# Kernel optimization log

Hardware: AMD Instinct MI355X
Metric: run time of the kernel (lower is better)

The kernel has to match this reference:

```python
import jax, jax.numpy as jnp
import numpy as np

EPS = 1e-10

def setup_inputs() -> dict:
    key = jax.random.key(0)
    k1, k2 = jax.random.split(key)
    B, N, D = 8, 4096, 3
    points_ref = jax.random.normal(k1, (B, N, D), dtype=jnp.float32)
    points = jax.random.normal(k2, (B, N, D), dtype=jnp.float32)
    return {"points_ref": points_ref, "points": points, "nn_size": 16}

def _knn(points_ref, K):
    # pairwise squared distances (B,N,N)
    sq = jnp.sum(points_ref * points_ref, axis=-1)
    d2 = sq[:, :, None] + sq[:, None, :] - 2.0 * jnp.einsum('bnd,bmd->bnm', points_ref, points_ref)
    _, idx = jax.lax.top_k(-d2, K)  # nearest first; idx: (B,N,K)
    return idx

def reference(points_ref, points, nn_size):
    K = nn_size + 1
    knn_idx = _knn(points_ref, K)[:, :, 1:]  # drop self -> (B,N,nn_size)
    gather = jax.vmap(lambda p, i: p[i])  # (N,D),(N,K) -> (N,K,D)
    group_ref = gather(points_ref, knn_idx)           # (B,N,K,D)
    group_pred = gather(points, knn_idx)              # (B,N,K,D)
    dist_ref = jnp.linalg.norm(group_ref - points_ref[:, :, None, :], axis=-1)  # (B,N,K)
    dist = jnp.linalg.norm(group_pred - points[:, :, None, :], axis=-1)         # (B,N,K)
    stretch = jnp.maximum(dist / (dist_ref + EPS) - 1.0, 0.0)
    return jnp.mean(stretch)
```

## Files before the change

### kernel.cpp

```cpp
#include <hip/hip_runtime.h>

#define NPTS  4096
#define KNN   16
#define K1    17
#define NBLK  64
#define CELLS 4096
#define EPSF  1e-10f

__device__ __forceinline__ unsigned umin_(unsigned a, unsigned b) { return a < b ? a : b; }
__device__ __forceinline__ unsigned umax_(unsigned a, unsigned b) { return a < b ? b : a; }

#define DPP_XOR1(v)  ((unsigned)__builtin_amdgcn_update_dpp(0, (int)(v), 0xB1, 0xF, 0xF, true))
#define DPP_XOR2(v)  ((unsigned)__builtin_amdgcn_update_dpp(0, (int)(v), 0x4E, 0xF, 0xF, true))
#define SWZ_XOR(v,J) ((unsigned)__builtin_amdgcn_ds_swizzle((int)(v), ((J) << 10) | 0x1F))
#define DPP_SHR1(v)  ((unsigned)__builtin_amdgcn_update_dpp(0, (int)(v), 0x111, 0xF, 0xF, true))
#define DPPF_SHR(vf, CTRL) __uint_as_float((unsigned)__builtin_amdgcn_update_dpp(0, (int)__float_as_uint(vf), CTRL, 0xF, 0xF, true))
#define LXOR1(v)  DPP_XOR1(v)
#define LXOR2(v)  DPP_XOR2(v)
#define LXOR4(v)  SWZ_XOR(v, 4)
#define LXOR8(v)  SWZ_XOR(v, 8)
#define LXOR16(v) SWZ_XOR(v, 16)
#define LXOR32(v) ((unsigned)__shfl_xor((int)(v), 32))

#define BSTEP(K, XORF) do {                                                   \
    unsigned o1_ = XORF(arr), o2_ = XORF(bk);                                 \
    bool tm_ = (((lane & (J_)) == 0) == ((lane & (K)) == 0));                 \
    unsigned mn1_ = umin_(arr, o1_), mx1_ = umax_(arr, o1_);                  \
    unsigned mn2_ = umin_(bk, o2_),  mx2_ = umax_(bk, o2_);                   \
    arr = tm_ ? mn1_ : mx1_; bk = tm_ ? mn2_ : mx2_;                          \
} while (0)

__device__ __forceinline__ unsigned sp4(int v) {
    unsigned x = (unsigned)v;
    return (x & 1u) | ((x & 2u) << 2) | ((x & 4u) << 4) | ((x & 8u) << 6);
}

__global__ __launch_bounds__(1024) void sort_kernel(
    const float* __restrict__ pref,
    float4* __restrict__ wxyzw, int* __restrict__ widx, float4* __restrict__ wbb)
{
    __shared__ unsigned hist[CELLS];
    __shared__ unsigned short cells[NPTS];
    __shared__ unsigned wofs[16];
    const int tid  = threadIdx.x;
    const int lane = tid & 63, w = tid >> 6;
    const int b = blockIdx.x;
    const float* prb = pref + (size_t)b * NPTS * 3;
    const size_t base = (size_t)b * NPTS;

    for (int t = tid; t < CELLS; t += 1024) hist[t] = 0u;
    __syncthreads();

    for (int p = tid; p < NPTS; p += 1024) {
        float x = prb[3 * p + 0], y = prb[3 * p + 1], z = prb[3 * p + 2];
        int cx = min(15, max(0, (int)((x + 4.0f) * 2.0f)));
        int cy = min(15, max(0, (int)((y + 4.0f) * 2.0f)));
        int cz = min(15, max(0, (int)((z + 4.0f) * 2.0f)));
        unsigned m = sp4(cx) | (sp4(cy) << 1) | (sp4(cz) << 2);
        cells[p] = (unsigned short)m;
        atomicAdd(&hist[m], 1u);
    }
    __syncthreads();

    unsigned l0 = hist[4 * tid + 0], l1 = hist[4 * tid + 1];
    unsigned l2 = hist[4 * tid + 2], l3 = hist[4 * tid + 3];
    unsigned s = l0 + l1 + l2 + l3;
    unsigned run = s;
#pragma unroll
    for (int d = 1; d < 64; d <<= 1) {
        unsigned o = __shfl_up(run, d);
        if (lane >= d) run += o;
    }
    if (lane == 63) wofs[w] = run;
    __syncthreads();
    if (tid == 0) {
        unsigned acc = 0;
#pragma unroll
        for (int k = 0; k < 16; ++k) { unsigned t2 = wofs[k]; wofs[k] = acc; acc += t2; }
    }
    __syncthreads();
    unsigned excl = wofs[w] + run - s;
    hist[4 * tid + 0] = excl;
    hist[4 * tid + 1] = excl + l0;
    hist[4 * tid + 2] = excl + l0 + l1;
    hist[4 * tid + 3] = excl + l0 + l1 + l2;
    __syncthreads();

    for (int p = tid; p < NPTS; p += 1024) {
        unsigned c = cells[p];
        unsigned pos = atomicAdd(&hist[c], 1u);
        wxyzw[base + pos] = make_float4(prb[3 * p + 0], prb[3 * p + 1], prb[3 * p + 2], 0.f);
        widx[base + pos]  = p;
    }
    __syncthreads();

#pragma unroll
    for (int rep = 0; rep < 4; ++rep) {
        int blk = w + rep * 16;
        float4 c = wxyzw[base + blk * 64 + lane];
        float mnx = c.x, mxx = c.x, mny = c.y, mxy2 = c.y, mnz = c.z, mxz = c.z;
#pragma unroll
        for (int d = 32; d > 0; d >>= 1) {
            mnx  = fminf(mnx,  __shfl_xor(mnx,  d));
            mxx  = fmaxf(mxx,  __shfl_xor(mxx,  d));
            mny  = fminf(mny,  __shfl_xor(mny,  d));
            mxy2 = fmaxf(mxy2, __shfl_xor(mxy2, d));
            mnz  = fminf(mnz,  __shfl_xor(mnz,  d));
            mxz  = fmaxf(mxz,  __shfl_xor(mxz,  d));
        }
        if (lane == 0) {
            wbb[((size_t)b * NBLK + blk) * 2 + 0] = make_float4(mnx, mny, mnz, 0.f);
            wbb[((size_t)b * NBLK + blk) * 2 + 1] = make_float4(mxx, mxy2, mxz, 0.f);
        }
    }
}

#define EVENTS(KEY) do {                                                      \
    unsigned long long m_ = __ballot((KEY) < thr);                            \
    if (m_) {                                                                 \
        do {                                                                  \
            int l_ = __ffsll(m_) - 1;                                         \
            m_ &= m_ - 1;                                                     \
            unsigned kk_ = (unsigned)__builtin_amdgcn_readlane((int)(KEY), l_);\
            unsigned long long lt_ = __ballot(arr < kk_) & 0x1FFFFull;        \
            int pos_ = __popcll(lt_);                                         \
            unsigned up_ = DPP_SHR1(arr);                                     \
            unsigned a15_ = (unsigned)__builtin_amdgcn_readlane((int)arr, 15);\
            up_ = (lane == 16) ? a15_ : up_;                                  \
            arr = (lane == pos_) ? kk_ : ((lane > pos_) ? up_ : arr);         \
        } while (m_);                                                         \
        thr = (unsigned)__builtin_amdgcn_readlane((int)arr, K1 - 1);          \
    } } while (0)

__global__ __launch_bounds__(256, 8) void knn_main_kernel(
    const float* __restrict__ ppred,
    const float4* __restrict__ wxyzw, const int* __restrict__ widx,
    const float4* __restrict__ wbb, float* __restrict__ partials, int NQ)
{
    const int lane = threadIdx.x & 63;
    const int wv   = blockIdx.x * 4 + (threadIdx.x >> 6);
    const int q = ((NQ & (NQ - 1)) == 0) ? (int)(((unsigned)wv * 26765u) & (unsigned)(NQ - 1)) : wv;

    const int b = q >> 12;
    const int p = q & (NPTS - 1);
    const size_t base = (size_t)b * NPTS;
    const int p0 = p & ~63, ownblk = p >> 6;

    const float4 qc = wxyzw[base + p];
    const float qx = qc.x, qy = qc.y, qz = qc.z;

    unsigned arr;
    {
        float4 c = wxyzw[base + p0 + lane];
        float dx = c.x - qx, dy = c.y - qy, dz = c.z - qz;
        float d2 = dx * dx + dy * dy + dz * dz;
        arr = (__float_as_uint(d2) & 0xFFFFF000u) | (unsigned)(p0 + lane);
    }
    unsigned bk;
    {
        float4 mn4 = wbb[((size_t)b * NBLK + lane) * 2 + 0];
        float4 mx4 = wbb[((size_t)b * NBLK + lane) * 2 + 1];
        float ddx = fmaxf(fmaxf(mn4.x - qx, qx - mx4.x), 0.0f);
        float ddy = fmaxf(fmaxf(mn4.y - qy, qy - mx4.y), 0.0f);
        float ddz = fmaxf(fmaxf(mn4.z - qz, qz - mx4.z), 0.0f);
        float bd2 = ddx * ddx + ddy * ddy + ddz * ddz;
        bk = (__float_as_uint(bd2) & 0xFFFFF000u) | (unsigned)lane;
        bk = (lane == ownblk) ? 0xFFFFFFFFu : bk;
    }

    {
        int J_;
        J_ = 1;  BSTEP(2,  LXOR1);
        J_ = 2;  BSTEP(4,  LXOR2);  J_ = 1; BSTEP(4,  LXOR1);
        J_ = 4;  BSTEP(8,  LXOR4);  J_ = 2; BSTEP(8,  LXOR2);  J_ = 1; BSTEP(8,  LXOR1);
        J_ = 8;  BSTEP(16, LXOR8);  J_ = 4; BSTEP(16, LXOR4);  J_ = 2; BSTEP(16, LXOR2);  J_ = 1; BSTEP(16, LXOR1);
        J_ = 16; BSTEP(32, LXOR16); J_ = 8; BSTEP(32, LXOR8);  J_ = 4; BSTEP(32, LXOR4);  J_ = 2; BSTEP(32, LXOR2); J_ = 1; BSTEP(32, LXOR1);
        J_ = 32; BSTEP(64, LXOR32); J_ = 16; BSTEP(64, LXOR16); J_ = 8; BSTEP(64, LXOR8); J_ = 4; BSTEP(64, LXOR4); J_ = 2; BSTEP(64, LXOR2); J_ = 1; BSTEP(64, LXOR1);
    }
    unsigned thr = (unsigned)__builtin_amdgcn_readlane((int)arr, K1 - 1);

    int k = 0;
    unsigned bcur = (unsigned)__builtin_amdgcn_readlane((int)bk, 0);
    bool have = (bcur < thr);
    float4 cur;
    if (have) cur = wxyzw[base + (int)(bcur & 0xFFFu) * 64 + lane];
    while (have) {
        unsigned bnext = (unsigned)__builtin_amdgcn_readlane((int)bk, k + 1);
        bool pf = (bnext < thr);
        float4 nxt;
        if (pf) nxt = wxyzw[base + (int)(bnext & 0xFFFu) * 64 + lane];
        int jbase = (int)(bcur & 0xFFFu) * 64;
        float dx = cur.x - qx, dy = cur.y - qy, dz = cur.z - qz;
        float d2 = dx * dx + dy * dy + dz * dz;
        unsigned key = (__float_as_uint(d2) & 0xFFFFF000u) | (unsigned)(jbase + lane);
        EVENTS(key);
        ++k;
        bcur = bnext;
        have = (bcur < thr);
        cur = nxt;
    }

    const float* ppb = ppred + (size_t)b * NPTS * 3;
    const int iorig = widx[base + p];
    float s = 0.f;
    if (lane >= 1 && lane <= KNN) {
        int js = (int)(arr & 0xFFFu);
        float4 rc = wxyzw[base + js];
        float rx = rc.x - qx, ry = rc.y - qy, rz = rc.z - qz;
        float dref = sqrtf(rx * rx + ry * ry + rz * rz);
        int nj = widx[base + js];
        float px = ppb[3 * iorig + 0], py = ppb[3 * iorig + 1], pz = ppb[3 * iorig + 2];
        float ax = ppb[3 * nj + 0] - px;
        float ay = ppb[3 * nj + 1] - py;
        float az = ppb[3 * nj + 2] - pz;
        float dpred = sqrtf(ax * ax + ay * ay + az * az);
        s = fmaxf(dpred / (dref + EPSF) - 1.0f, 0.0f);
    }
    s += DPPF_SHR(s, 0x111);
    s += DPPF_SHR(s, 0x112);
    s += DPPF_SHR(s, 0x114);
    s += DPPF_SHR(s, 0x118);
    float t15 = __uint_as_float((unsigned)__builtin_amdgcn_readlane((int)__float_as_uint(s), 15));
    float t16 = __uint_as_float((unsigned)__builtin_amdgcn_readlane((int)__float_as_uint(s), 16));
    if (lane == 0) partials[q] = t15 + t16;
}

__global__ __launch_bounds__(1024) void reduce_kernel(
    const float* __restrict__ partials, int n, float* __restrict__ out, float scale)
{
    __shared__ float wsum[16];
    float s = 0.f;
    for (int idx = threadIdx.x; idx < n; idx += 1024) s += partials[idx];
    for (int off = 32; off > 0; off >>= 1) s += __shfl_down(s, off);
    if ((threadIdx.x & 63) == 0) wsum[threadIdx.x >> 6] = s;
    __syncthreads();
    if (threadIdx.x == 0) {
        float t = 0.f;
#pragma unroll
        for (int k = 0; k < 16; ++k) t += wsum[k];
        out[0] = t * scale;
    }
}

extern "C" void kernel_launch(void* const* d_in, const int* in_sizes, int n_in,
                              void* d_out, int out_size, void* d_ws, size_t ws_size,
                              hipStream_t stream) {
    const float* pref  = (const float*)d_in[0];
    const float* ppred = (const float*)d_in[1];
    float* out = (float*)d_out;

    const int B  = in_sizes[0] / (NPTS * 3);
    const int NQ = B * NPTS;
    const float scale = 1.0f / ((float)NQ * (float)KNN);

    char* ws = (char*)d_ws;
    float4* wxyzw = (float4*)ws;
    int*    widx  = (int*)   (ws + (size_t)B * NPTS * 16);
    float4* wbb   = (float4*)(ws + (size_t)B * NPTS * 20);
    float*  partials = (float*)(ws + (size_t)B * NPTS * 20 + (size_t)B * NBLK * 32);

    sort_kernel<<<dim3(B), dim3(1024), 0, stream>>>(pref, wxyzw, widx, wbb);
    knn_main_kernel<<<dim3(NQ / 4), dim3(256), 0, stream>>>(ppred, wxyzw, widx, wbb, partials, NQ);
    reduce_kernel<<<dim3(1), dim3(1024), 0, stream>>>(partials, NQ, out, scale);
}
```

Baseline: 74.78 us.

## Fuse final reduction into knn kernel via atomics and use DPP for bbox reductions

Removes the separate single-block reduce kernel by having each knn block reduce its four wave sums in shared memory and atomically add the scaled value into the output, which is zeroed by a memset. This swaps a kernel launch and the partials round-trip for 8192 global atomics on one address plus a memset node. The bounding-box min/max reductions in the sort kernel also switch from __shfl_xor to DPP and swizzle lane exchanges. Float atomic ordering makes the final sum nondeterministic.

```diff
diff --git a/kernel.cpp b/kernel.cpp
--- a/kernel.cpp
+++ b/kernel.cpp
@@ -9,6 +9,9 @@
 
 __device__ __forceinline__ unsigned umin_(unsigned a, unsigned b) { return a < b ? a : b; }
 __device__ __forceinline__ unsigned umax_(unsigned a, unsigned b) { return a < b ? b : a; }
+__device__ __forceinline__ unsigned rdlane(unsigned v, int l) {
+    return (unsigned)__builtin_amdgcn_readlane((int)v, l);
+}
 
 #define DPP_XOR1(v)  ((unsigned)__builtin_amdgcn_update_dpp(0, (int)(v), 0xB1, 0xF, 0xF, true))
 #define DPP_XOR2(v)  ((unsigned)__builtin_amdgcn_update_dpp(0, (int)(v), 0x4E, 0xF, 0xF, true))
@@ -21,6 +24,15 @@
 #define LXOR8(v)  SWZ_XOR(v, 8)
 #define LXOR16(v) SWZ_XOR(v, 16)
 #define LXOR32(v) ((unsigned)__shfl_xor((int)(v), 32))
+
+#define FXMIN(a, XORF) do {                                                   \
+    unsigned o_ = XORF(__float_as_uint(a));                                   \
+    a = fminf(a, __uint_as_float(o_));                                        \
+} while (0)
+#define FXMAX(a, XORF) do {                                                   \
+    unsigned o_ = XORF(__float_as_uint(a));                                   \
+    a = fmaxf(a, __uint_as_float(o_));                                        \
+} while (0)
 
 #define BSTEP(K, XORF) do {                                                   \
     unsigned o1_ = XORF(arr), o2_ = XORF(bk);                                 \
@@ -99,15 +111,18 @@
         int blk = w + rep * 16;
         float4 c = wxyzw[base + blk * 64 + lane];
         float mnx = c.x, mxx = c.x, mny = c.y, mxy2 = c.y, mnz = c.z, mxz = c.z;
-#pragma unroll
-        for (int d = 32; d > 0; d >>= 1) {
-            mnx  = fminf(mnx,  __shfl_xor(mnx,  d));
-            mxx  = fmaxf(mxx,  __shfl_xor(mxx,  d));
-            mny  = fminf(mny,  __shfl_xor(mny,  d));
-            mxy2 = fmaxf(mxy2, __shfl_xor(mxy2, d));
-            mnz  = fminf(mnz,  __shfl_xor(mnz,  d));
-            mxz  = fmaxf(mxz,  __shfl_xor(mxz,  d));
-        }
+        FXMIN(mnx, LXOR1);  FXMAX(mxx, LXOR1);  FXMIN(mny, LXOR1);
+        FXMAX(mxy2, LXOR1); FXMIN(mnz, LXOR1);  FXMAX(mxz, LXOR1);
+        FXMIN(mnx, LXOR2);  FXMAX(mxx, LXOR2);  FXMIN(mny, LXOR2);
+        FXMAX(mxy2, LXOR2); FXMIN(mnz, LXOR2);  FXMAX(mxz, LXOR2);
+        FXMIN(mnx, LXOR4);  FXMAX(mxx, LXOR4);  FXMIN(mny, LXOR4);
+        FXMAX(mxy2, LXOR4); FXMIN(mnz, LXOR4);  FXMAX(mxz, LXOR4);
+        FXMIN(mnx, LXOR8);  FXMAX(mxx, LXOR8);  FXMIN(mny, LXOR8);
+        FXMAX(mxy2, LXOR8); FXMIN(mnz, LXOR8);  FXMAX(mxz, LXOR8);
+        FXMIN(mnx, LXOR16); FXMAX(mxx, LXOR16); FXMIN(mny, LXOR16);
+        FXMAX(mxy2, LXOR16); FXMIN(mnz, LXOR16); FXMAX(mxz, LXOR16);
+        FXMIN(mnx, LXOR32); FXMAX(mxx, LXOR32); FXMIN(mny, LXOR32);
+        FXMAX(mxy2, LXOR32); FXMIN(mnz, LXOR32); FXMAX(mxz, LXOR32);
         if (lane == 0) {
             wbb[((size_t)b * NBLK + blk) * 2 + 0] = make_float4(mnx, mny, mnz, 0.f);
             wbb[((size_t)b * NBLK + blk) * 2 + 1] = make_float4(mxx, mxy2, mxz, 0.f);
@@ -121,22 +136,23 @@
         do {                                                                  \
             int l_ = __ffsll(m_) - 1;                                         \
             m_ &= m_ - 1;                                                     \
-            unsigned kk_ = (unsigned)__builtin_amdgcn_readlane((int)(KEY), l_);\
+            unsigned kk_ = rdlane(KEY, l_);                                   \
             unsigned long long lt_ = __ballot(arr < kk_) & 0x1FFFFull;        \
             int pos_ = __popcll(lt_);                                         \
             unsigned up_ = DPP_SHR1(arr);                                     \
-            unsigned a15_ = (unsigned)__builtin_amdgcn_readlane((int)arr, 15);\
+            unsigned a15_ = rdlane(arr, 15);                                  \
             up_ = (lane == 16) ? a15_ : up_;                                  \
             arr = (lane == pos_) ? kk_ : ((lane > pos_) ? up_ : arr);         \
         } while (m_);                                                         \
-        thr = (unsigned)__builtin_amdgcn_readlane((int)arr, K1 - 1);          \
+        thr = rdlane(arr, K1 - 1);                                            \
     } } while (0)
 
 __global__ __launch_bounds__(256, 8) void knn_main_kernel(
     const float* __restrict__ ppred,
     const float4* __restrict__ wxyzw, const int* __restrict__ widx,
-    const float4* __restrict__ wbb, float* __restrict__ partials, int NQ)
+    const float4* __restrict__ wbb, float* __restrict__ out, float scale, int NQ)
 {
+    __shared__ float wsum[4];
     const int lane = threadIdx.x & 63;
     const int wv   = blockIdx.x * 4 + (threadIdx.x >> 6);
     const int q = ((NQ & (NQ - 1)) == 0) ? (int)(((unsigned)wv * 26765u) & (unsigned)(NQ - 1)) : wv;
@@ -177,15 +193,15 @@
         J_ = 16; BSTEP(32, LXOR16); J_ = 8; BSTEP(32, LXOR8);  J_ = 4; BSTEP(32, LXOR4);  J_ = 2; BSTEP(32, LXOR2); J_ = 1; BSTEP(32, LXOR1);
         J_ = 32; BSTEP(64, LXOR32); J_ = 16; BSTEP(64, LXOR16); J_ = 8; BSTEP(64, LXOR8); J_ = 4; BSTEP(64, LXOR4); J_ = 2; BSTEP(64, LXOR2); J_ = 1; BSTEP(64, LXOR1);
     }
-    unsigned thr = (unsigned)__builtin_amdgcn_readlane((int)arr, K1 - 1);
+    unsigned thr = rdlane(arr, K1 - 1);
 
     int k = 0;
-    unsigned bcur = (unsigned)__builtin_amdgcn_readlane((int)bk, 0);
+    unsigned bcur = rdlane(bk, 0);
     bool have = (bcur < thr);
     float4 cur;
     if (have) cur = wxyzw[base + (int)(bcur & 0xFFFu) * 64 + lane];
     while (have) {
-        unsigned bnext = (unsigned)__builtin_amdgcn_readlane((int)bk, k + 1);
+        unsigned bnext = rdlane(bk, k + 1);
         bool pf = (bnext < thr);
         float4 nxt;
         if (pf) nxt = wxyzw[base + (int)(bnext & 0xFFFu) * 64 + lane];
@@ -220,26 +236,13 @@
     s += DPPF_SHR(s, 0x112);
     s += DPPF_SHR(s, 0x114);
     s += DPPF_SHR(s, 0x118);
-    float t15 = __uint_as_float((unsigned)__builtin_amdgcn_readlane((int)__float_as_uint(s), 15));
-    float t16 = __uint_as_float((unsigned)__builtin_amdgcn_readlane((int)__float_as_uint(s), 16));
-    if (lane == 0) partials[q] = t15 + t16;
-}
-
-__global__ __launch_bounds__(1024) void reduce_kernel(
-    const float* __restrict__ partials, int n, float* __restrict__ out, float scale)
-{
-    __shared__ float wsum[16];
-    float s = 0.f;
-    for (int idx = threadIdx.x; idx < n; idx += 1024) s += partials[idx];
-    for (int off = 32; off > 0; off >>= 1) s += __shfl_down(s, off);
-    if ((threadIdx.x & 63) == 0) wsum[threadIdx.x >> 6] = s;
-    __syncthreads();
-    if (threadIdx.x == 0) {
-        float t = 0.f;
-#pragma unroll
-        for (int k = 0; k < 16; ++k) t += wsum[k];
-        out[0] = t * scale;
-    }
+    float t15 = __uint_as_float(rdlane(__float_as_uint(s), 15));
+    float t16 = __uint_as_float(rdlane(__float_as_uint(s), 16));
+
+    if (lane == 0) wsum[threadIdx.x >> 6] = t15 + t16;
+    __syncthreads();
+    if (threadIdx.x == 0)
+        atomicAdd(out, ((wsum[0] + wsum[1]) + (wsum[2] + wsum[3])) * scale);
 }
 
 extern "C" void kernel_launch(void* const* d_in, const int* in_sizes, int n_in,
@@ -257,9 +260,8 @@
     float4* wxyzw = (float4*)ws;
     int*    widx  = (int*)   (ws + (size_t)B * NPTS * 16);
     float4* wbb   = (float4*)(ws + (size_t)B * NPTS * 20);
-    float*  partials = (float*)(ws + (size_t)B * NPTS * 20 + (size_t)B * NBLK * 32);
-
+
+    hipMemsetAsync(d_out, 0, sizeof(float), stream);
     sort_kernel<<<dim3(B), dim3(1024), 0, stream>>>(pref, wxyzw, widx, wbb);
-    knn_main_kernel<<<dim3(NQ / 4), dim3(256), 0, stream>>>(ppred, wxyzw, widx, wbb, partials, NQ);
-    reduce_kernel<<<dim3(1), dim3(1024), 0, stream>>>(partials, NQ, out, scale);
-}
+    knn_main_kernel<<<dim3(NQ / 4), dim3(256), 0, stream>>>(ppred, wxyzw, widx, wbb, out, scale, NQ);
+}
```

Result: slower. 136.3 us (+82.3%).

## Process four neighboring queries per wave sharing candidate block traversal

Applied to the files above, without the earlier changes.

Each wavefront now handles four spatially adjacent queries, sharing the initial own-block distance computation, the bitonic sort of block keys, and each candidate block load across all four. Block traversal is ordered by the first query's box distance and terminated with a triangle-inequality bound using the group radius. This amortizes sorting and memory traffic per query, at the cost of more registers, serialized per-query insertion loops, and a looser pruning bound that can visit more blocks.

```diff
diff --git a/kernel.cpp b/kernel.cpp
--- a/kernel.cpp
+++ b/kernel.cpp
@@ -9,6 +9,9 @@
 
 __device__ __forceinline__ unsigned umin_(unsigned a, unsigned b) { return a < b ? a : b; }
 __device__ __forceinline__ unsigned umax_(unsigned a, unsigned b) { return a < b ? b : a; }
+__device__ __forceinline__ unsigned rdlane(unsigned v, int l) {
+    return (unsigned)__builtin_amdgcn_readlane((int)v, l);
+}
 
 #define DPP_XOR1(v)  ((unsigned)__builtin_amdgcn_update_dpp(0, (int)(v), 0xB1, 0xF, 0xF, true))
 #define DPP_XOR2(v)  ((unsigned)__builtin_amdgcn_update_dpp(0, (int)(v), 0x4E, 0xF, 0xF, true))
@@ -22,12 +25,15 @@
 #define LXOR16(v) SWZ_XOR(v, 16)
 #define LXOR32(v) ((unsigned)__shfl_xor((int)(v), 32))
 
-#define BSTEP(K, XORF) do {                                                   \
-    unsigned o1_ = XORF(arr), o2_ = XORF(bk);                                 \
+#define BSTEP5(K, XORF) do {                                                  \
+    unsigned o0_ = XORF(arr0), o1_ = XORF(arr1);                              \
+    unsigned o2_ = XORF(arr2), o3_ = XORF(arr3), ob_ = XORF(bk);              \
     bool tm_ = (((lane & (J_)) == 0) == ((lane & (K)) == 0));                 \
-    unsigned mn1_ = umin_(arr, o1_), mx1_ = umax_(arr, o1_);                  \
-    unsigned mn2_ = umin_(bk, o2_),  mx2_ = umax_(bk, o2_);                   \
-    arr = tm_ ? mn1_ : mx1_; bk = tm_ ? mn2_ : mx2_;                          \
+    arr0 = tm_ ? umin_(arr0, o0_) : umax_(arr0, o0_);                         \
+    arr1 = tm_ ? umin_(arr1, o1_) : umax_(arr1, o1_);                         \
+    arr2 = tm_ ? umin_(arr2, o2_) : umax_(arr2, o2_);                         \
+    arr3 = tm_ ? umin_(arr3, o3_) : umax_(arr3, o3_);                         \
+    bk   = tm_ ? umin_(bk,   ob_) : umax_(bk,   ob_);                         \
 } while (0)
 
 __device__ __forceinline__ unsigned sp4(int v) {
@@ -115,54 +121,112 @@
     }
 }
 
-#define EVENTS(KEY) do {                                                      \
-    unsigned long long m_ = __ballot((KEY) < thr);                            \
+#define EVQ(KEY, ARR, THR) do {                                               \
+    unsigned long long m_ = __ballot((KEY) < THR);                            \
     if (m_) {                                                                 \
         do {                                                                  \
             int l_ = __ffsll(m_) - 1;                                         \
             m_ &= m_ - 1;                                                     \
-            unsigned kk_ = (unsigned)__builtin_amdgcn_readlane((int)(KEY), l_);\
-            unsigned long long lt_ = __ballot(arr < kk_) & 0x1FFFFull;        \
+            unsigned kk_ = rdlane(KEY, l_);                                   \
+            unsigned long long lt_ = __ballot(ARR < kk_) & 0x1FFFFull;        \
             int pos_ = __popcll(lt_);                                         \
-            unsigned up_ = DPP_SHR1(arr);                                     \
-            unsigned a15_ = (unsigned)__builtin_amdgcn_readlane((int)arr, 15);\
+            unsigned up_ = DPP_SHR1(ARR);                                     \
+            unsigned a15_ = rdlane(ARR, 15);                                  \
             up_ = (lane == 16) ? a15_ : up_;                                  \
-            arr = (lane == pos_) ? kk_ : ((lane > pos_) ? up_ : arr);         \
+            ARR = (lane == pos_) ? kk_ : ((lane > pos_) ? up_ : ARR);         \
         } while (m_);                                                         \
-        thr = (unsigned)__builtin_amdgcn_readlane((int)arr, K1 - 1);          \
+        THR = rdlane(ARR, K1 - 1);                                            \
     } } while (0)
+
+#define THRUP(T) sqrtf(__uint_as_float(((T) & 0xFFFFF000u) + 0x1000u))
+#define LIMIT()  (fmaxf(fmaxf(THRUP(thr0), THRUP(thr1)),                      \
+                        fmaxf(THRUP(thr2), THRUP(thr3))) + D0)
+
+#define EPI(ARR, P, QX, QY, QZ) do {                                          \
+    const int iorig_ = widx[base + (P)];                                      \
+    float s_ = 0.f;                                                           \
+    if (lane >= 1 && lane <= KNN) {                                           \
+        int js_ = (int)((ARR) & 0xFFFu);                                      \
+        float4 rc_ = wxyzw[base + js_];                                       \
+        float rx_ = rc_.x - (QX), ry_ = rc_.y - (QY), rz_ = rc_.z - (QZ);     \
+        float dref_ = sqrtf(rx_ * rx_ + ry_ * ry_ + rz_ * rz_);               \
+        int nj_ = widx[base + js_];                                           \
+        float px_ = ppb[3 * iorig_ + 0], py_ = ppb[3 * iorig_ + 1], pz_ = ppb[3 * iorig_ + 2]; \
+        float ax_ = ppb[3 * nj_ + 0] - px_;                                   \
+        float ay_ = ppb[3 * nj_ + 1] - py_;                                   \
+        float az_ = ppb[3 * nj_ + 2] - pz_;                                   \
+        float dpred_ = sqrtf(ax_ * ax_ + ay_ * ay_ + az_ * az_);              \
+        s_ = fmaxf(dpred_ / (dref_ + EPSF) - 1.0f, 0.0f);                     \
+    }                                                                         \
+    s_ += DPPF_SHR(s_, 0x111);                                                \
+    s_ += DPPF_SHR(s_, 0x112);                                                \
+    s_ += DPPF_SHR(s_, 0x114);                                                \
+    s_ += DPPF_SHR(s_, 0x118);                                                \
+    acc += __uint_as_float(rdlane(__float_as_uint(s_), 15))                   \
+         + __uint_as_float(rdlane(__float_as_uint(s_), 16));                  \
+} while (0)
 
 __global__ __launch_bounds__(256, 8) void knn_main_kernel(
     const float* __restrict__ ppred,
     const float4* __restrict__ wxyzw, const int* __restrict__ widx,
-    const float4* __restrict__ wbb, float* __restrict__ partials, int NQ)
+    const float4* __restrict__ wbb, float* __restrict__ partials, int NG)
 {
     const int lane = threadIdx.x & 63;
     const int wv   = blockIdx.x * 4 + (threadIdx.x >> 6);
-    const int q = ((NQ & (NQ - 1)) == 0) ? (int)(((unsigned)wv * 26765u) & (unsigned)(NQ - 1)) : wv;
-
-    const int b = q >> 12;
-    const int p = q & (NPTS - 1);
+    const int g = ((NG & (NG - 1)) == 0) ? (int)(((unsigned)wv * 26765u) & (unsigned)(NG - 1)) : wv;
+
+    const int q0id = g * 4;
+    const int b  = q0id >> 12;
+    const int p0 = q0id & (NPTS - 1);
+    const int p1 = p0 + 1, p2 = p0 + 2, p3 = p0 + 3;
     const size_t base = (size_t)b * NPTS;
-    const int p0 = p & ~63, ownblk = p >> 6;
-
-    const float4 qc = wxyzw[base + p];
-    const float qx = qc.x, qy = qc.y, qz = qc.z;
-
-    unsigned arr;
+    const int pblk = p0 & ~63, ownblk = p0 >> 6;
+
+    const float4 qc0 = wxyzw[base + p0];
+    const float4 qc1 = wxyzw[base + p1];
+    const float4 qc2 = wxyzw[base + p2];
+    const float4 qc3 = wxyzw[base + p3];
+    const float qx0 = qc0.x, qy0 = qc0.y, qz0 = qc0.z;
+    const float qx1 = qc1.x, qy1 = qc1.y, qz1 = qc1.z;
+    const float qx2 = qc2.x, qy2 = qc2.y, qz2 = qc2.z;
+    const float qx3 = qc3.x, qy3 = qc3.y, qz3 = qc3.z;
+
+    float D0;
     {
-        float4 c = wxyzw[base + p0 + lane];
-        float dx = c.x - qx, dy = c.y - qy, dz = c.z - qz;
-        float d2 = dx * dx + dy * dy + dz * dz;
-        arr = (__float_as_uint(d2) & 0xFFFFF000u) | (unsigned)(p0 + lane);
+        float ax = qx1 - qx0, ay = qy1 - qy0, az = qz1 - qz0;
+        float bx = qx2 - qx0, by = qy2 - qy0, bz = qz2 - qz0;
+        float cx = qx3 - qx0, cy = qy3 - qy0, cz = qz3 - qz0;
+        float da = ax * ax + ay * ay + az * az;
+        float db = bx * bx + by * by + bz * bz;
+        float dc = cx * cx + cy * cy + cz * cz;
+        D0 = sqrtf(fmaxf(fmaxf(da, db), dc));
+    }
+
+    unsigned arr0, arr1, arr2, arr3;
+    {
+        float4 c = wxyzw[base + pblk + lane];
+        unsigned jj = (unsigned)(pblk + lane);
+        float dx, dy, dz, d2;
+        dx = c.x - qx0; dy = c.y - qy0; dz = c.z - qz0;
+        d2 = dx * dx + dy * dy + dz * dz;
+        arr0 = (__float_as_uint(d2) & 0xFFFFF000u) | jj;
+        dx = c.x - qx1; dy = c.y - qy1; dz = c.z - qz1;
+        d2 = dx * dx + dy * dy + dz * dz;
+        arr1 = (__float_as_uint(d2) & 0xFFFFF000u) | jj;
+        dx = c.x - qx2; dy = c.y - qy2; dz = c.z - qz2;
+        d2 = dx * dx + dy * dy + dz * dz;
+        arr2 = (__float_as_uint(d2) & 0xFFFFF000u) | jj;
+        dx = c.x - qx3; dy = c.y - qy3; dz = c.z - qz3;
+        d2 = dx * dx + dy * dy + dz * dz;
+        arr3 = (__float_as_uint(d2) & 0xFFFFF000u) | jj;
     }
     unsigned bk;
     {
         float4 mn4 = wbb[((size_t)b * NBLK + lane) * 2 + 0];
         float4 mx4 = wbb[((size_t)b * NBLK + lane) * 2 + 1];
-        float ddx = fmaxf(fmaxf(mn4.x - qx, qx - mx4.x), 0.0f);
-        float ddy = fmaxf(fmaxf(mn4.y - qy, qy - mx4.y), 0.0f);
-        float ddz = fmaxf(fmaxf(mn4.z - qz, qz - mx4.z), 0.0f);
+        float ddx = fmaxf(fmaxf(mn4.x - qx0, qx0 - mx4.x), 0.0f);
+        float ddy = fmaxf(fmaxf(mn4.y - qy0, qy0 - mx4.y), 0.0f);
+        float ddz = fmaxf(fmaxf(mn4.z - qz0, qz0 - mx4.z), 0.0f);
         float bd2 = ddx * ddx + ddy * ddy + ddz * ddz;
         bk = (__float_as_uint(bd2) & 0xFFFFF000u) | (unsigned)lane;
         bk = (lane == ownblk) ? 0xFFFFFFFFu : bk;
@@ -170,59 +234,70 @@
 
     {
         int J_;
-        J_ = 1;  BSTEP(2,  LXOR1);
-        J_ = 2;  BSTEP(4,  LXOR2);  J_ = 1; BSTEP(4,  LXOR1);
-        J_ = 4;  BSTEP(8,  LXOR4);  J_ = 2; BSTEP(8,  LXOR2);  J_ = 1; BSTEP(8,  LXOR1);
-        J_ = 8;  BSTEP(16, LXOR8);  J_ = 4; BSTEP(16, LXOR4);  J_ = 2; BSTEP(16, LXOR2);  J_ = 1; BSTEP(16, LXOR1);
-        J_ = 16; BSTEP(32, LXOR16); J_ = 8; BSTEP(32, LXOR8);  J_ = 4; BSTEP(32, LXOR4);  J_ = 2; BSTEP(32, LXOR2); J_ = 1; BSTEP(32, LXOR1);
-        J_ = 32; BSTEP(64, LXOR32); J_ = 16; BSTEP(64, LXOR16); J_ = 8; BSTEP(64, LXOR8); J_ = 4; BSTEP(64, LXOR4); J_ = 2; BSTEP(64, LXOR2); J_ = 1; BSTEP(64, LXOR1);
-    }
-    unsigned thr = (unsigned)__builtin_amdgcn_readlane((int)arr, K1 - 1);
-
+        J_ = 1;  BSTEP5(2,  LXOR1);
+        J_ = 2;  BSTEP5(4,  LXOR2);  J_ = 1; BSTEP5(4,  LXOR1);
+        J_ = 4;  BSTEP5(8,  LXOR4);  J_ = 2; BSTEP5(8,  LXOR2);  J_ = 1; BSTEP5(8,  LXOR1);
+        J_ = 8;  BSTEP5(16, LXOR8);  J_ = 4; BSTEP5(16, LXOR4);  J_ = 2; BSTEP5(16, LXOR2);  J_ = 1; BSTEP5(16, LXOR1);
+        J_ = 16; BSTEP5(32, LXOR16); J_ = 8; BSTEP5(32, LXOR8);  J_ = 4; BSTEP5(32, LXOR4);  J_ = 2; BSTEP5(32, LXOR2); J_ = 1; BSTEP5(32, LXOR1);
+        J_ = 32; BSTEP5(64, LXOR32); J_ = 16; BSTEP5(64, LXOR16); J_ = 8; BSTEP5(64, LXOR8); J_ = 4; BSTEP5(64, LXOR4); J_ = 2; BSTEP5(64, LXOR2); J_ = 1; BSTEP5(64, LXOR1);
+    }
+    unsigned thr0 = rdlane(arr0, K1 - 1);
+    unsigned thr1 = rdlane(arr1, K1 - 1);
+    unsigned thr2 = rdlane(arr2, K1 - 1);
+    unsigned thr3 = rdlane(arr3, K1 - 1);
+
+    float limit = LIMIT();
     int k = 0;
-    unsigned bcur = (unsigned)__builtin_amdgcn_readlane((int)bk, 0);
-    bool have = (bcur < thr);
+    unsigned bcur = rdlane(bk, 0);
+    float bd = sqrtf(__uint_as_float(bcur & 0xFFFFF000u));
+    bool have = (bd < limit);
     float4 cur;
     if (have) cur = wxyzw[base + (int)(bcur & 0xFFFu) * 64 + lane];
     while (have) {
-        unsigned bnext = (unsigned)__builtin_amdgcn_readlane((int)bk, k + 1);
-        bool pf = (bnext < thr);
+        unsigned bnext = rdlane(bk, k + 1);
+        float bdn = sqrtf(__uint_as_float(bnext & 0xFFFFF000u));
+        bool pf = (bdn < limit);
         float4 nxt;
         if (pf) nxt = wxyzw[base + (int)(bnext & 0xFFFu) * 64 + lane];
-        int jbase = (int)(bcur & 0xFFFu) * 64;
-        float dx = cur.x - qx, dy = cur.y - qy, dz = cur.z - qz;
-        float d2 = dx * dx + dy * dy + dz * dz;
-        unsigned key = (__float_as_uint(d2) & 0xFFFFF000u) | (unsigned)(jbase + lane);
-        EVENTS(key);
+        unsigned j = (unsigned)((int)(bcur & 0xFFFu) * 64 + lane);
+        {
+            float dx = cur.x - qx0, dy = cur.y - qy0, dz = cur.z - qz0;
+            float d2 = dx * dx + dy * dy + dz * dz;
+            unsigned key = (__float_as_uint(d2) & 0xFFFFF000u) | j;
+            EVQ(key, arr0, thr0);
+        }
+        {
+            float dx = cur.x - qx1, dy = cur.y - qy1, dz = cur.z - qz1;
+            float d2 = dx * dx + dy * dy + dz * dz;
+            unsigned key = (__float_as_uint(d2) & 0xFFFFF000u) | j;
+            EVQ(key, arr1, thr1);
+        }
+        {
+            float dx = cur.x - qx2, dy = cur.y - qy2, dz = cur.z - qz2;
+            float d2 = dx * dx + dy * dy + dz * dz;
+            unsigned key = (__float_as_uint(d2) & 0xFFFFF000u) | j;
+            EVQ(key, arr2, thr2);
+        }
+        {
+            float dx = cur.x - qx3, dy = cur.y - qy3, dz = cur.z - qz3;
+            float d2 = dx * dx + dy * dy + dz * dz;
+            unsigned key = (__float_as_uint(d2) & 0xFFFFF000u) | j;
+            EVQ(key, arr3, thr3);
+        }
+        limit = LIMIT();
         ++k;
         bcur = bnext;
-        have = (bcur < thr);
+        have = pf && (bdn < limit);
         cur = nxt;
     }
 
     const float* ppb = ppred + (size_t)b * NPTS * 3;
-    const int iorig = widx[base + p];
-    float s = 0.f;
-    if (lane >= 1 && lane <= KNN) {
-        int js = (int)(arr & 0xFFFu);
-        float4 rc = wxyzw[base + js];
-        float rx = rc.x - qx, ry = rc.y - qy, rz = rc.z - qz;
-        float dref = sqrtf(rx * rx + ry * ry + rz * rz);
-        int nj = widx[base + js];
-        float px = ppb[3 * iorig + 0], py = ppb[3 * iorig + 1], pz = ppb[3 * iorig + 2];
-        float ax = ppb[3 * nj + 0] - px;
-        float ay = ppb[3 * nj + 1] - py;
-        float az = ppb[3 * nj + 2] - pz;
-        float dpred = sqrtf(ax * ax + ay * ay + az * az);
-        s = fmaxf(dpred / (dref + EPSF) - 1.0f, 0.0f);
-    }
-    s += DPPF_SHR(s, 0x111);
-    s += DPPF_SHR(s, 0x112);
-    s += DPPF_SHR(s, 0x114);
-    s += DPPF_SHR(s, 0x118);
-    float t15 = __uint_as_float((unsigned)__builtin_amdgcn_readlane((int)__float_as_uint(s), 15));
-    float t16 = __uint_as_float((unsigned)__builtin_amdgcn_readlane((int)__float_as_uint(s), 16));
-    if (lane == 0) partials[q] = t15 + t16;
+    float acc = 0.f;
+    EPI(arr0, p0, qx0, qy0, qz0);
+    EPI(arr1, p1, qx1, qy1, qz1);
+    EPI(arr2, p2, qx2, qy2, qz2);
+    EPI(arr3, p3, qx3, qy3, qz3);
+    if (lane == 0) partials[wv] = acc;
 }
 
 __global__ __launch_bounds__(1024) void reduce_kernel(
@@ -251,6 +326,7 @@
 
     const int B  = in_sizes[0] / (NPTS * 3);
     const int NQ = B * NPTS;
+    const int NG = NQ / 4;
     const float scale = 1.0f / ((float)NQ * (float)KNN);
 
     char* ws = (char*)d_ws;
@@ -260,6 +336,6 @@
     float*  partials = (float*)(ws + (size_t)B * NPTS * 20 + (size_t)B * NBLK * 32);
 
     sort_kernel<<<dim3(B), dim3(1024), 0, stream>>>(pref, wxyzw, widx, wbb);
-    knn_main_kernel<<<dim3(NQ / 4), dim3(256), 0, stream>>>(ppred, wxyzw, widx, wbb, partials, NQ);
-    reduce_kernel<<<dim3(1), dim3(1024), 0, stream>>>(partials, NQ, out, scale);
-}
+    knn_main_kernel<<<dim3(NG / 4), dim3(256), 0, stream>>>(ppred, wxyzw, widx, wbb, partials, NG);
+    reduce_kernel<<<dim3(1), dim3(1024), 0, stream>>>(partials, NG, out, scale);
+}
```

Result: slower. 132.7 us (+77.4%).
